# Performance work log

Hardware: AMD Instinct MI355X
Metric: run time of the kernel (lower is better)

Reference implementation:

```python
import jax, jax.numpy as jnp
import numpy as np

N = 100000   # num nodes
E = 500000   # num hyperedges
NNZ = 1600000
H, C = 4, 32
IN_CH = 128


def setup_inputs() -> dict:
    key = jax.random.key(0)
    k1, k2, k3, k4, k5 = jax.random.split(key, 5)
    X = jax.random.normal(k1, (N, IN_CH), dtype=jnp.float32)
    W = jax.random.normal(k2, (IN_CH, H * C), dtype=jnp.float32) * (1.0 / np.sqrt(IN_CH))
    att_e = jax.random.normal(k3, (1, H, C), dtype=jnp.float32) * 0.1
    vertex = jax.random.randint(k4, (NNZ,), 0, N, dtype=jnp.int64)
    edges = jax.random.randint(k5, (NNZ,), 0, E, dtype=jnp.int64)
    return {"X": X, "W": W, "att_e": att_e, "vertex": vertex, "edges": edges}


def reference(X, W, att_e, vertex, edges):
    n = X.shape[0]
    X0 = X @ W                                  # [N, H*C]
    Xh = X0.reshape(n, H, C)                    # [N, H, C]
    Xve = Xh[vertex]                            # [nnz, H, C] gather
    # scatter-mean over hyperedges
    esum = jax.ops.segment_sum(Xve, edges, num_segments=E)            # [E, H, C]
    cnt = jax.ops.segment_sum(jnp.ones((Xve.shape[0],), X.dtype), edges, num_segments=E)
    Xe = esum / jnp.maximum(cnt, 1.0)[:, None, None]                  # [E, H, C]
    # per-edge attention score
    alpha_e = (Xe * att_e).sum(-1)              # [E, H]
    a_ev = alpha_e[edges]                       # [nnz, H]
    alpha = jax.nn.leaky_relu(a_ev, 0.01)
    # segment softmax over vertex groups
    m = jax.ops.segment_max(alpha, vertex, num_segments=n)            # [N, H]
    ex = jnp.exp(alpha - m[vertex])
    den = jax.ops.segment_sum(ex, vertex, num_segments=n)             # [N, H]
    alpha = ex / (den[vertex] + 1e-16)          # [nnz, H]
    # weighted scatter-sum back to nodes
    Xev = Xe[edges] * alpha[:, :, None]         # [nnz, H, C]
    Xv = jax.ops.segment_sum(Xev, vertex, num_segments=n)             # [N, H, C]
    return Xv.reshape(n, H * C) + X0
```

## Files before the change

kernel.cpp:

```cpp
#include <hip/hip_runtime.h>
#include <hip/hip_bf16.h>
#include <hip/hip_fp16.h>
#include <cstdint>

#define NH 4
#define HC 128
#define INCH 128
#define NEDGE 500000
#define NN 100000

#define KE_SHIFT 11
#define KV_SHIFT 9
#define KE (1 << KE_SHIFT)
#define KV (1 << KV_SHIFT)
#define NBE 245
#define NBV 196
#define CAP_E 8192
#define CAP_V 10240
#define CHUNK_A 8192

typedef float          f32x2 __attribute__((ext_vector_type(2)));
typedef float          f32x4 __attribute__((ext_vector_type(4)));
typedef float          f32x8 __attribute__((ext_vector_type(8)));
typedef unsigned int   u32x2 __attribute__((ext_vector_type(2)));
typedef unsigned int   u32x4 __attribute__((ext_vector_type(4)));
typedef unsigned short u16x8 __attribute__((ext_vector_type(8)));

static __device__ __forceinline__ unsigned short f2bf(float f){
  union { float f; unsigned u; } v; v.f = f;
  unsigned r = v.u + 0x7fffu + ((v.u >> 16) & 1u);
  return (unsigned short)(r >> 16);
}
static __device__ __forceinline__ float bf2f(unsigned short b){
  union { unsigned u; float f; } v; v.u = ((unsigned)b) << 16;
  return v.f;
}
static __device__ __forceinline__ f32x8 bf8f(u16x8 b){
  f32x8 r;
  r[0]=bf2f(b[0]); r[1]=bf2f(b[1]); r[2]=bf2f(b[2]); r[3]=bf2f(b[3]);
  r[4]=bf2f(b[4]); r[5]=bf2f(b[5]); r[6]=bf2f(b[6]); r[7]=bf2f(b[7]);
  return r;
}

#if __has_builtin(__builtin_amdgcn_cvt_pk_fp8_f32) && __has_builtin(__builtin_amdgcn_cvt_pk_f32_fp8)
#define FP8_HW 1
#else
#define FP8_HW 0
#endif

#if !FP8_HW
static __device__ __forceinline__ unsigned enc1_fp8(float v){
  union{ __half h; unsigned short u; } c; c.h = __float2half(v);
  unsigned u = c.u;
  unsigned s = (u>>15)&1u, e=(u>>10)&31u, m=u&0x3FFu;
  int e8 = (int)e - 8;
  unsigned lsb = (m>>7)&1u;
  unsigned m8 = (m + 63u + lsb) >> 7;
  if (m8 == 8u){ m8 = 0u; e8 += 1; }
  if (e8 <= 0)  return s<<7;
  if (e8 >= 16) return (s<<7)|0x7Eu;
  return (s<<7)|((unsigned)e8<<3)|m8;
}
static __device__ __forceinline__ float dec1_fp8(unsigned b){
  unsigned s=(b>>7)&1u, e=(b>>3)&15u, m=b&7u;
  union{unsigned u; float f;} r;
  if (e==0u){ r.f = (float)m * 0.001953125f; if(s) r.f = -r.f; }
  else r.u = (s<<31)|((e+120u)<<23)|(m<<20);
  return r.f;
}
#endif

static __device__ __forceinline__ u32x2 pack8_fp8(const f32x8 v){
  u32x2 w;
#if FP8_HW
  int w0 = __builtin_amdgcn_cvt_pk_fp8_f32(v[0], v[1], 0, false);
  w0     = __builtin_amdgcn_cvt_pk_fp8_f32(v[2], v[3], w0, true);
  int w1 = __builtin_amdgcn_cvt_pk_fp8_f32(v[4], v[5], 0, false);
  w1     = __builtin_amdgcn_cvt_pk_fp8_f32(v[6], v[7], w1, true);
  w.x = (unsigned)w0; w.y = (unsigned)w1;
#else
  w.x = enc1_fp8(v[0]) | (enc1_fp8(v[1])<<8) | (enc1_fp8(v[2])<<16) | (enc1_fp8(v[3])<<24);
  w.y = enc1_fp8(v[4]) | (enc1_fp8(v[5])<<8) | (enc1_fp8(v[6])<<16) | (enc1_fp8(v[7])<<24);
#endif
  return w;
}
static __device__ __forceinline__ void fma8s_fp8(f32x8& acc, float c, float w, u32x2 q){
#if FP8_HW
  f32x2 p;
  p = __builtin_amdgcn_cvt_pk_f32_fp8((int)q.x, false); acc[0]=acc[0]*c + w*p.x; acc[1]=acc[1]*c + w*p.y;
  p = __builtin_amdgcn_cvt_pk_f32_fp8((int)q.x, true ); acc[2]=acc[2]*c + w*p.x; acc[3]=acc[3]*c + w*p.y;
  p = __builtin_amdgcn_cvt_pk_f32_fp8((int)q.y, false); acc[4]=acc[4]*c + w*p.x; acc[5]=acc[5]*c + w*p.y;
  p = __builtin_amdgcn_cvt_pk_f32_fp8((int)q.y, true ); acc[6]=acc[6]*c + w*p.x; acc[7]=acc[7]*c + w*p.y;
#else
  acc[0]=acc[0]*c + w*dec1_fp8(q.x&0xFF);        acc[1]=acc[1]*c + w*dec1_fp8((q.x>>8)&0xFF);
  acc[2]=acc[2]*c + w*dec1_fp8((q.x>>16)&0xFF);  acc[3]=acc[3]*c + w*dec1_fp8(q.x>>24);
  acc[4]=acc[4]*c + w*dec1_fp8(q.y&0xFF);        acc[5]=acc[5]*c + w*dec1_fp8((q.y>>8)&0xFF);
  acc[6]=acc[6]*c + w*dec1_fp8((q.y>>16)&0xFF);  acc[7]=acc[7]*c + w*dec1_fp8(q.y>>24);
#endif
}

#define GBM 128
#define GBK 16
__global__ __launch_bounds__(256) void gemm_x0(const float* __restrict__ X,
                                               const float* __restrict__ Wm,
                                               const float* __restrict__ att,
                                               unsigned short* __restrict__ X0bf,
                                               float* __restrict__ score, int nrows){
  __shared__ float As[GBK][GBM+4];
  __shared__ float Bs[GBK][HC+4];
  __shared__ float sc[GBM][17];
  const int tid  = threadIdx.x;
  const int row0 = blockIdx.x * GBM;
  const int trow = tid >> 4;
  const int tcol = tid & 15;
  float acc[8][8];
  #pragma unroll
  for (int i=0;i<8;i++)
    #pragma unroll
    for (int j=0;j<8;j++) acc[i][j]=0.f;

  for (int k0=0;k0<INCH;k0+=GBK){
    #pragma unroll
    for (int l = tid; l < 512; l += 256){
      int r  = l >> 2;
      int ks = (l & 3) * 4;
      int grow = row0 + r;
      float4 v = make_float4(0.f,0.f,0.f,0.f);
      if (grow < nrows) v = *(const float4*)(X + (size_t)grow*INCH + k0 + ks);
      As[ks+0][r]=v.x; As[ks+1][r]=v.y; As[ks+2][r]=v.z; As[ks+3][r]=v.w;
    }
    #pragma unroll
    for (int l = tid; l < 512; l += 256){
      int r  = l >> 5;
      int cs = (l & 31) * 4;
      float4 v = *(const float4*)(Wm + (size_t)(k0+r)*HC + cs);
      *(float4*)(&Bs[r][cs]) = v;
    }
    __syncthreads();
    #pragma unroll
    for (int kk=0;kk<GBK;kk++){
      float a[8], b[8];
      *(float4*)&a[0] = *(float4*)&As[kk][trow*8];
      *(float4*)&a[4] = *(float4*)&As[kk][trow*8+4];
      *(float4*)&b[0] = *(float4*)&Bs[kk][tcol*8];
      *(float4*)&b[4] = *(float4*)&Bs[kk][tcol*8+4];
      #pragma unroll
      for (int i=0;i<8;i++)
        #pragma unroll
        for (int j=0;j<8;j++) acc[i][j] = fmaf(a[i], b[j], acc[i][j]);
    }
    __syncthreads();
  }
  float attv[8];
  *(float4*)&attv[0] = *(const float4*)(att + tcol*8);
  *(float4*)&attv[4] = *(const float4*)(att + tcol*8 + 4);
  #pragma unroll
  for (int i=0;i<8;i++){
    int grow = row0 + trow*8 + i;
    float p = 0.f;
    #pragma unroll
    for (int j=0;j<8;j++) p = fmaf(acc[i][j], attv[j], p);
    sc[trow*8+i][tcol] = p;
    if (grow < nrows){
      ushort4 b0, b1;
      b0.x=f2bf(acc[i][0]); b0.y=f2bf(acc[i][1]); b0.z=f2bf(acc[i][2]); b0.w=f2bf(acc[i][3]);
      b1.x=f2bf(acc[i][4]); b1.y=f2bf(acc[i][5]); b1.z=f2bf(acc[i][6]); b1.w=f2bf(acc[i][7]);
      *(ushort4*)(X0bf + (size_t)grow*HC + tcol*8    ) = b0;
      *(ushort4*)(X0bf + (size_t)grow*HC + tcol*8 + 4) = b1;
    }
  }
  __syncthreads();
  for (int idx = tid; idx < GBM*NH; idx += 256){
    int row = idx >> 2, h = idx & 3;
    int grow = row0 + row;
    if (grow < nrows){
      float s = sc[row][4*h] + sc[row][4*h+1] + sc[row][4*h+2] + sc[row][4*h+3];
      score[(size_t)grow*NH + h] = s;
    }
  }
}

__global__ __launch_bounds__(512) void phaseA(const int* __restrict__ vertex,
                                              const int* __restrict__ edges, int nnz,
                                              int* __restrict__ cursE, int* __restrict__ cursV,
                                              unsigned* __restrict__ stgE, unsigned* __restrict__ stgV){
  __shared__ int cE[NBE], c2E[NBE], gE[NBE];
  __shared__ int cV[NBV], c2V[NBV], gV[NBV];
  const int t = threadIdx.x;
  const int base = blockIdx.x * CHUNK_A;
  int ev[16], vv[16];
  #pragma unroll
  for (int j=0;j<16;j++){
    int i = base + t + j*512;
    if (i < nnz){ ev[j] = edges[i]; vv[j] = vertex[i]; }
    else ev[j] = -1;
  }
  for (int j=t;j<NBE;j+=512){ cE[j]=0; c2E[j]=0; }
  for (int j=t;j<NBV;j+=512){ cV[j]=0; c2V[j]=0; }
  __syncthreads();
  #pragma unroll
  for (int j=0;j<16;j++) if (ev[j]>=0){
    atomicAdd(&cE[ev[j]>>KE_SHIFT], 1);
    atomicAdd(&cV[vv[j]>>KV_SHIFT], 1);
  }
  __syncthreads();
  for (int j=t;j<NBE;j+=512) gE[j] = atomicAdd(&cursE[j], cE[j]);
  for (int j=t;j<NBV;j+=512) gV[j] = atomicAdd(&cursV[j], cV[j]);
  __syncthreads();
  #pragma unroll
  for (int j=0;j<16;j++) if (ev[j]>=0){
    int bE = ev[j]>>KE_SHIFT;
    int p = gE[bE] + atomicAdd(&c2E[bE],1);
    if (p < CAP_E) stgE[(size_t)bE*CAP_E + p] = ((unsigned)vv[j] << KE_SHIFT) | (unsigned)(ev[j] & (KE-1));
    int bV = vv[j]>>KV_SHIFT;
    int q = gV[bV] + atomicAdd(&c2V[bV],1);
    if (q < CAP_V) stgV[(size_t)bV*CAP_V + q] = ((unsigned)ev[j] << KV_SHIFT) | (unsigned)(vv[j] & (KV-1));
  }
}

template<int K, int CAP, int IT, int SHIFT, int NB>
__device__ __forceinline__ void phaseB_body(const unsigned* __restrict__ stg,
                                            const int* __restrict__ curs,
                                            int* __restrict__ offsOut,
                                            int* __restrict__ csrOut, int nKeys, int b,
                                            int* cur, int* tsum, int* bsh){
  const int t = threadIdx.x;
  const int k0 = b * K;
  const int kc = min(K, nKeys - k0);
  int c = (t < NB) ? min(curs[t], CAP) : 0;
  bsh[t] = c; __syncthreads();
  for (int d2=1; d2<512; d2<<=1){
    int x = (t>=d2) ? bsh[t-d2] : 0; __syncthreads();
    bsh[t] += x; __syncthreads();
  }
  const int gbase = (b > 0) ? bsh[b-1] : 0;
  const int cnt   = min(curs[b], CAP);
  if (b == NB-1 && t == 0) offsOut[nKeys] = bsh[NB-1];
  unsigned it[IT];
  #pragma unroll
  for (int j=0;j<IT;j++){
    int i = t + j*512;
    it[j] = (i < cnt) ? stg[(size_t)b*CAP + i] : 0xFFFFFFFFu;
  }
  for (int j=t;j<K;j+=512) cur[j] = 0;
  __syncthreads();
  #pragma unroll
  for (int j=0;j<IT;j++) if (it[j] != 0xFFFFFFFFu) atomicAdd(&cur[it[j] & (K-1)], 1);
  __syncthreads();
  constexpr int KPT = K / 512;
  int loc[KPT]; int s = 0;
  #pragma unroll
  for (int j=0;j<KPT;j++){ loc[j] = s; s += cur[t*KPT + j]; }
  tsum[t] = s; __syncthreads();
  for (int d2=1; d2<512; d2<<=1){
    int x = (t>=d2) ? tsum[t-d2] : 0; __syncthreads();
    tsum[t] += x; __syncthreads();
  }
  const int tbase = tsum[t] - s;
  __syncthreads();
  #pragma unroll
  for (int j=0;j<KPT;j++){
    int k = t*KPT + j;
    int abs0 = gbase + tbase + loc[j];
    if (k < kc) offsOut[k0 + k] = abs0;
    cur[k] = abs0;
  }
  __syncthreads();
  #pragma unroll
  for (int j=0;j<IT;j++) if (it[j] != 0xFFFFFFFFu){
    int pos = atomicAdd(&cur[it[j] & (K-1)], 1);
    csrOut[pos] = (int)(it[j] >> SHIFT);
  }
}

__global__ __launch_bounds__(512) void phaseB_fused(const unsigned* __restrict__ stgE,
                                                    const unsigned* __restrict__ stgV,
                                                    const int* __restrict__ cursE,
                                                    const int* __restrict__ cursV,
                                                    int* __restrict__ eoffs, int* __restrict__ voffs,
                                                    int* __restrict__ ecsr, int* __restrict__ vcsr){
  __shared__ int cur[KE];
  __shared__ int tsum[512];
  __shared__ int bsh[512];
  const int b = blockIdx.x;
  if (b < NBE) phaseB_body<KE, CAP_E, CAP_E/512, KE_SHIFT, NBE>(stgE, cursE, eoffs, ecsr, NEDGE, b, cur, tsum, bsh);
  else         phaseB_body<KV, CAP_V, CAP_V/512, KV_SHIFT, NBV>(stgV, cursV, voffs, vcsr, NN, b - NBE, cur, tsum, bsh);
}

__global__ __launch_bounds__(256) void edge_agg(const unsigned short* __restrict__ X0bf,
                                                const float* __restrict__ score,
                                                const int* __restrict__ ecsr,
                                                const int* __restrict__ eoffs,
                                                unsigned char* __restrict__ Xe8,
                                                unsigned* __restrict__ alphaS, int E){
  int eg = blockIdx.x * 16 + (threadIdx.x >> 4);
  if (eg >= E) return;
  const int lane  = threadIdx.x & 15;
  const int cbase = lane * 8;
  const int start = eoffs[eg];
  const int d     = eoffs[eg+1] - start;
  f32x8 acc0 = {0.f,0.f,0.f,0.f,0.f,0.f,0.f,0.f};
  f32x8 acc1 = {0.f,0.f,0.f,0.f,0.f,0.f,0.f,0.f};
  float sacc0 = 0.f, sacc1 = 0.f;
  int k = 0;
  for (; k+1<d; k+=2){
    int v0 = ecsr[start + k];
    int v1 = ecsr[start + k + 1];
    u16x8 x0 = *(const u16x8*)(X0bf + (size_t)v0*HC + cbase);
    u16x8 x1 = *(const u16x8*)(X0bf + (size_t)v1*HC + cbase);
    if (lane < NH){
      sacc0 += score[(size_t)v0*NH + lane];
      sacc1 += score[(size_t)v1*NH + lane];
    }
    acc0 += bf8f(x0);
    acc1 += bf8f(x1);
  }
  if (k < d){
    int v0 = ecsr[start + k];
    u16x8 x0 = *(const u16x8*)(X0bf + (size_t)v0*HC + cbase);
    if (lane < NH) sacc0 += score[(size_t)v0*NH + lane];
    acc0 += bf8f(x0);
  }
  acc0 += acc1;
  const float inv = 1.0f / fmaxf((float)d, 1.0f);
  acc0 *= inv;
  float lm = fmaxf(fmaxf(fmaxf(fabsf(acc0[0]),fabsf(acc0[1])),fmaxf(fabsf(acc0[2]),fabsf(acc0[3]))),
                   fmaxf(fmaxf(fabsf(acc0[4]),fabsf(acc0[5])),fmaxf(fabsf(acc0[6]),fabsf(acc0[7]))));
  #pragma unroll
  for (int s=1; s<16; s<<=1) lm = fmaxf(lm, __shfl_xor(lm, s, 16));
  const float qs  = (lm > 1e-30f) ? 448.0f/lm : 0.f;
  const float dqs = (lm > 1e-30f) ? lm*(1.0f/448.0f) : 0.f;
  f32x8 q = acc0 * qs;
  u32x2 w = pack8_fp8(q);
  *(u32x2*)(Xe8 + (size_t)eg*HC + cbase) = w;
  float aa = (sacc0 + sacc1) * inv;
  aa = aa > 0.f ? aa : 0.01f*aa;
  float a0 = __shfl(aa, 0, 16);
  float a1 = __shfl(aa, 1, 16);
  float a2 = __shfl(aa, 2, 16);
  float a3 = __shfl(aa, 3, 16);
  if (lane == 0){
    u32x4 rec;
    rec.x = (unsigned)__half_as_ushort(__float2half(a0)) | ((unsigned)__half_as_ushort(__float2half(a1)) << 16);
    rec.y = (unsigned)__half_as_ushort(__float2half(a2)) | ((unsigned)__half_as_ushort(__float2half(a3)) << 16);
    rec.z = __float_as_uint(dqs);
    rec.w = 0u;
    *(u32x4*)(alphaS + (size_t)eg*4) = rec;
  }
}

__global__ __launch_bounds__(256) void vert_pass(const unsigned short* __restrict__ X0bf,
                                                 const unsigned char* __restrict__ Xe8,
                                                 const unsigned* __restrict__ alphaS,
                                                 const int* __restrict__ vcsr,
                                                 const int* __restrict__ voffs,
                                                 float* __restrict__ out, int N){
  int n = blockIdx.x * 16 + (threadIdx.x >> 4);
  if (n >= N) return;
  const int lane  = threadIdx.x & 15;
  const int cbase = lane * 8;
  const int h     = lane >> 2;
  const size_t obase = (size_t)n*HC + cbase;
  f32x8 x0 = bf8f(*(const u16x8*)(X0bf + obase));
  const int start = voffs[n];
  const int d     = voffs[n+1] - start;
  if (d == 0){
    f32x4 lo = {x0[0],x0[1],x0[2],x0[3]}, hi = {x0[4],x0[5],x0[6],x0[7]};
    __builtin_nontemporal_store(lo, (f32x4*)(out + obase));
    __builtin_nontemporal_store(hi, (f32x4*)(out + obase + 4));
    return;
  }

  float m0=-1e30f, m1=-1e30f, m2=-1e30f, m3=-1e30f;
  float den0=0.f, den1=0.f, den2=0.f, den3=0.f;
  f32x8 acc0 = {0.f,0.f,0.f,0.f,0.f,0.f,0.f,0.f};
  f32x8 acc1 = {0.f,0.f,0.f,0.f,0.f,0.f,0.f,0.f};
  f32x8 acc2 = {0.f,0.f,0.f,0.f,0.f,0.f,0.f,0.f};
  f32x8 acc3 = {0.f,0.f,0.f,0.f,0.f,0.f,0.f,0.f};

#define EXTRACT(rec, aval, sval) { \
    unsigned word_ = (h < 2) ? (rec).x : (rec).y; \
    unsigned h16_  = (h & 1) ? (word_ >> 16) : (word_ & 0xFFFFu); \
    aval = __half2float(__ushort_as_half((unsigned short)h16_)); \
    sval = __uint_as_float((rec).z); }

#define UPD(i, rec, q) { \
    float a_, s_; EXTRACT(rec, a_, s_); \
    float mn_ = fmaxf(m##i, a_); \
    float c_  = __expf(m##i - mn_); \
    float p_  = __expf(a_ - mn_); \
    den##i = den##i * c_ + p_; \
    fma8s_fp8(acc##i, c_, p_ * s_, (q)); \
    m##i = mn_; }

  int k = 0;
  for (; k+3<d; k+=4){
    int e0 = vcsr[start + k];
    int e1 = vcsr[start + k + 1];
    int e2 = vcsr[start + k + 2];
    int e3 = vcsr[start + k + 3];
    u32x4 r0 = *(const u32x4*)(alphaS + (size_t)e0*4);
    u32x4 r1 = *(const u32x4*)(alphaS + (size_t)e1*4);
    u32x4 r2 = *(const u32x4*)(alphaS + (size_t)e2*4);
    u32x4 r3 = *(const u32x4*)(alphaS + (size_t)e3*4);
    u32x2 q0 = *(const u32x2*)(Xe8 + (size_t)e0*HC + cbase);
    u32x2 q1 = *(const u32x2*)(Xe8 + (size_t)e1*HC + cbase);
    u32x2 q2 = *(const u32x2*)(Xe8 + (size_t)e2*HC + cbase);
    u32x2 q3 = *(const u32x2*)(Xe8 + (size_t)e3*HC + cbase);
    UPD(0, r0, q0);
    UPD(1, r1, q1);
    UPD(2, r2, q2);
    UPD(3, r3, q3);
  }
  for (; k<d; k++){
    int e0 = vcsr[start + k];
    u32x4 r0 = *(const u32x4*)(alphaS + (size_t)e0*4);
    u32x2 q0 = *(const u32x2*)(Xe8 + (size_t)e0*HC + cbase);
    UPD(0, r0, q0);
  }
#undef UPD
#undef EXTRACT

  float mn = fmaxf(fmaxf(m0,m1), fmaxf(m2,m3));
  float c0 = __expf(m0-mn), c1 = __expf(m1-mn), c2 = __expf(m2-mn), c3 = __expf(m3-mn);
  float den = den0*c0 + den1*c1 + den2*c2 + den3*c3;
  f32x8 acc = acc0*c0 + acc1*c1 + acc2*c2 + acc3*c3;
  const float w = 1.0f / (den + 1e-16f);
  acc = acc*w + x0;
  f32x4 lo = {acc[0],acc[1],acc[2],acc[3]};
  f32x4 hi = {acc[4],acc[5],acc[6],acc[7]};
  __builtin_nontemporal_store(lo, (f32x4*)(out + obase));
  __builtin_nontemporal_store(hi, (f32x4*)(out + obase + 4));
}

extern "C" void kernel_launch(void* const* d_in, const int* in_sizes, int n_in,
                              void* d_out, int out_size, void* d_ws, size_t ws_size,
                              hipStream_t stream){
  const float* X   = (const float*)d_in[0];
  const float* Wm  = (const float*)d_in[1];
  const float* att = (const float*)d_in[2];
  const int* vertex = (const int*)d_in[3];
  const int* edges  = (const int*)d_in[4];
  const int N   = in_sizes[0] / INCH;
  const int NNZ = in_sizes[3];
  const int E   = NEDGE;

  char* ws = (char*)d_ws;
  size_t off = 0;
  auto alloc = [&](size_t bytes)->char*{
    char* p = ws + off;
    off += (bytes + 255) & ~(size_t)255;
    return p;
  };
  unsigned char*  Xe8    = (unsigned char*)alloc((size_t)E * HC);
  unsigned short* X0bf   = (unsigned short*)alloc((size_t)NN * HC * sizeof(unsigned short));
  float*          score  = (float*)alloc((size_t)NN * NH * sizeof(float));
  unsigned*       alphaS = (unsigned*)alloc((size_t)E * 4 * sizeof(unsigned));
  int*            eoffs  = (int*)alloc((size_t)(E+1) * sizeof(int));
  int*            voffs  = (int*)alloc((size_t)(NN+1) * sizeof(int));
  int*            ecsr   = (int*)alloc((size_t)NNZ * sizeof(int));
  int*            vcsr   = (int*)alloc((size_t)NNZ * sizeof(int));
  int*            curs   = (int*)alloc((size_t)(NBE + NBV) * sizeof(int));
  int*            cursE  = curs;
  int*            cursV  = curs + NBE;
  unsigned* stgE = (unsigned*)(void*)Xe8;
  unsigned* stgV = (unsigned*)((char*)(void*)Xe8 + (size_t)NBE * CAP_E * sizeof(unsigned));

  hipMemsetAsync(curs, 0, (size_t)(NBE + NBV) * sizeof(int), stream);
  gemm_x0<<<(N + GBM - 1)/GBM, 256, 0, stream>>>(X, Wm, att, X0bf, score, N);
  phaseA<<<(NNZ + CHUNK_A - 1)/CHUNK_A, 512, 0, stream>>>(vertex, edges, NNZ, cursE, cursV, stgE, stgV);
  phaseB_fused<<<NBE + NBV, 512, 0, stream>>>(stgE, stgV, cursE, cursV, eoffs, voffs, ecsr, vcsr);
  edge_agg<<<(E + 15)/16, 256, 0, stream>>>(X0bf, score, ecsr, eoffs, Xe8, alphaS, E);
  vert_pass<<<(N + 15)/16, 256, 0, stream>>>(X0bf, Xe8, alphaS, vcsr, voffs, (float*)d_out, N);
}
```

Before: 260.6 us.

## Compute edge attention from aggregated features and drop online softmax max tracking

The per-node attention score is no longer computed in the GEMM epilogue. Each edge's score is now the dot product of its mean-aggregated features with att, reduced with shuffles, so the score buffer and its per-vertex gathers go away. edge_agg stores exp(leaky_relu(score)) directly as fp16. vert_pass then just sums these weights instead of running an online softmax with running max and rescaling, which removes two exps and several multiplies per incidence. The trade-off is that skipping max subtraction can overflow fp16/fp32 if scores are large, so correctness relies on the scores staying moderate.

```diff
diff --git a/kernel.cpp b/kernel.cpp
--- a/kernel.cpp
+++ b/kernel.cpp
@@ -84,18 +84,18 @@
 #endif
   return w;
 }
-static __device__ __forceinline__ void fma8s_fp8(f32x8& acc, float c, float w, u32x2 q){
+static __device__ __forceinline__ void fma8_fp8(f32x8& acc, float c, u32x2 q){
 #if FP8_HW
   f32x2 p;
-  p = __builtin_amdgcn_cvt_pk_f32_fp8((int)q.x, false); acc[0]=acc[0]*c + w*p.x; acc[1]=acc[1]*c + w*p.y;
-  p = __builtin_amdgcn_cvt_pk_f32_fp8((int)q.x, true ); acc[2]=acc[2]*c + w*p.x; acc[3]=acc[3]*c + w*p.y;
-  p = __builtin_amdgcn_cvt_pk_f32_fp8((int)q.y, false); acc[4]=acc[4]*c + w*p.x; acc[5]=acc[5]*c + w*p.y;
-  p = __builtin_amdgcn_cvt_pk_f32_fp8((int)q.y, true ); acc[6]=acc[6]*c + w*p.x; acc[7]=acc[7]*c + w*p.y;
+  p = __builtin_amdgcn_cvt_pk_f32_fp8((int)q.x, false); acc[0] += c*p.x; acc[1] += c*p.y;
+  p = __builtin_amdgcn_cvt_pk_f32_fp8((int)q.x, true ); acc[2] += c*p.x; acc[3] += c*p.y;
+  p = __builtin_amdgcn_cvt_pk_f32_fp8((int)q.y, false); acc[4] += c*p.x; acc[5] += c*p.y;
+  p = __builtin_amdgcn_cvt_pk_f32_fp8((int)q.y, true ); acc[6] += c*p.x; acc[7] += c*p.y;
 #else
-  acc[0]=acc[0]*c + w*dec1_fp8(q.x&0xFF);        acc[1]=acc[1]*c + w*dec1_fp8((q.x>>8)&0xFF);
-  acc[2]=acc[2]*c + w*dec1_fp8((q.x>>16)&0xFF);  acc[3]=acc[3]*c + w*dec1_fp8(q.x>>24);
-  acc[4]=acc[4]*c + w*dec1_fp8(q.y&0xFF);        acc[5]=acc[5]*c + w*dec1_fp8((q.y>>8)&0xFF);
-  acc[6]=acc[6]*c + w*dec1_fp8((q.y>>16)&0xFF);  acc[7]=acc[7]*c + w*dec1_fp8(q.y>>24);
+  acc[0] += c*dec1_fp8(q.x&0xFF);        acc[1] += c*dec1_fp8((q.x>>8)&0xFF);
+  acc[2] += c*dec1_fp8((q.x>>16)&0xFF);  acc[3] += c*dec1_fp8(q.x>>24);
+  acc[4] += c*dec1_fp8(q.y&0xFF);        acc[5] += c*dec1_fp8((q.y>>8)&0xFF);
+  acc[6] += c*dec1_fp8((q.y>>16)&0xFF);  acc[7] += c*dec1_fp8(q.y>>24);
 #endif
 }
 
@@ -103,12 +103,9 @@
 #define GBK 16
 __global__ __launch_bounds__(256) void gemm_x0(const float* __restrict__ X,
                                                const float* __restrict__ Wm,
-                                               const float* __restrict__ att,
-                                               unsigned short* __restrict__ X0bf,
-                                               float* __restrict__ score, int nrows){
+                                               unsigned short* __restrict__ X0bf, int nrows){
   __shared__ float As[GBK][GBM+4];
   __shared__ float Bs[GBK][HC+4];
-  __shared__ float sc[GBM][17];
   const int tid  = threadIdx.x;
   const int row0 = blockIdx.x * GBM;
   const int trow = tid >> 4;
@@ -151,31 +148,15 @@
     }
     __syncthreads();
   }
-  float attv[8];
-  *(float4*)&attv[0] = *(const float4*)(att + tcol*8);
-  *(float4*)&attv[4] = *(const float4*)(att + tcol*8 + 4);
   #pragma unroll
   for (int i=0;i<8;i++){
     int grow = row0 + trow*8 + i;
-    float p = 0.f;
-    #pragma unroll
-    for (int j=0;j<8;j++) p = fmaf(acc[i][j], attv[j], p);
-    sc[trow*8+i][tcol] = p;
     if (grow < nrows){
       ushort4 b0, b1;
       b0.x=f2bf(acc[i][0]); b0.y=f2bf(acc[i][1]); b0.z=f2bf(acc[i][2]); b0.w=f2bf(acc[i][3]);
       b1.x=f2bf(acc[i][4]); b1.y=f2bf(acc[i][5]); b1.z=f2bf(acc[i][6]); b1.w=f2bf(acc[i][7]);
       *(ushort4*)(X0bf + (size_t)grow*HC + tcol*8    ) = b0;
       *(ushort4*)(X0bf + (size_t)grow*HC + tcol*8 + 4) = b1;
-    }
-  }
-  __syncthreads();
-  for (int idx = tid; idx < GBM*NH; idx += 256){
-    int row = idx >> 2, h = idx & 3;
-    int grow = row0 + row;
-    if (grow < nrows){
-      float s = sc[row][4*h] + sc[row][4*h+1] + sc[row][4*h+2] + sc[row][4*h+3];
-      score[(size_t)grow*NH + h] = s;
     }
   }
 }
@@ -288,7 +269,7 @@
 }
 
 __global__ __launch_bounds__(256) void edge_agg(const unsigned short* __restrict__ X0bf,
-                                                const float* __restrict__ score,
+                                                const float* __restrict__ att,
                                                 const int* __restrict__ ecsr,
                                                 const int* __restrict__ eoffs,
                                                 unsigned char* __restrict__ Xe8,
@@ -297,33 +278,37 @@
   if (eg >= E) return;
   const int lane  = threadIdx.x & 15;
   const int cbase = lane * 8;
+  float attv[8];
+  *(f32x4*)&attv[0] = *(const f32x4*)(att + cbase);
+  *(f32x4*)&attv[4] = *(const f32x4*)(att + cbase + 4);
   const int start = eoffs[eg];
   const int d     = eoffs[eg+1] - start;
   f32x8 acc0 = {0.f,0.f,0.f,0.f,0.f,0.f,0.f,0.f};
   f32x8 acc1 = {0.f,0.f,0.f,0.f,0.f,0.f,0.f,0.f};
-  float sacc0 = 0.f, sacc1 = 0.f;
   int k = 0;
   for (; k+1<d; k+=2){
     int v0 = ecsr[start + k];
     int v1 = ecsr[start + k + 1];
     u16x8 x0 = *(const u16x8*)(X0bf + (size_t)v0*HC + cbase);
     u16x8 x1 = *(const u16x8*)(X0bf + (size_t)v1*HC + cbase);
-    if (lane < NH){
-      sacc0 += score[(size_t)v0*NH + lane];
-      sacc1 += score[(size_t)v1*NH + lane];
-    }
     acc0 += bf8f(x0);
     acc1 += bf8f(x1);
   }
   if (k < d){
     int v0 = ecsr[start + k];
     u16x8 x0 = *(const u16x8*)(X0bf + (size_t)v0*HC + cbase);
-    if (lane < NH) sacc0 += score[(size_t)v0*NH + lane];
     acc0 += bf8f(x0);
   }
   acc0 += acc1;
   const float inv = 1.0f / fmaxf((float)d, 1.0f);
   acc0 *= inv;
+  float p = 0.f;
+  #pragma unroll
+  for (int j=0;j<8;j++) p = fmaf(acc0[j], attv[j], p);
+  p += __shfl_xor(p, 1, 4);
+  p += __shfl_xor(p, 2, 4);
+  float a = p > 0.f ? p : 0.01f*p;
+  float e = __expf(a);
   float lm = fmaxf(fmaxf(fmaxf(fabsf(acc0[0]),fabsf(acc0[1])),fmaxf(fabsf(acc0[2]),fabsf(acc0[3]))),
                    fmaxf(fmaxf(fabsf(acc0[4]),fabsf(acc0[5])),fmaxf(fabsf(acc0[6]),fabsf(acc0[7]))));
   #pragma unroll
@@ -333,16 +318,14 @@
   f32x8 q = acc0 * qs;
   u32x2 w = pack8_fp8(q);
   *(u32x2*)(Xe8 + (size_t)eg*HC + cbase) = w;
-  float aa = (sacc0 + sacc1) * inv;
-  aa = aa > 0.f ? aa : 0.01f*aa;
-  float a0 = __shfl(aa, 0, 16);
-  float a1 = __shfl(aa, 1, 16);
-  float a2 = __shfl(aa, 2, 16);
-  float a3 = __shfl(aa, 3, 16);
+  float e0 = __shfl(e, 0, 16);
+  float e1 = __shfl(e, 4, 16);
+  float e2 = __shfl(e, 8, 16);
+  float e3 = __shfl(e, 12, 16);
   if (lane == 0){
     u32x4 rec;
-    rec.x = (unsigned)__half_as_ushort(__float2half(a0)) | ((unsigned)__half_as_ushort(__float2half(a1)) << 16);
-    rec.y = (unsigned)__half_as_ushort(__float2half(a2)) | ((unsigned)__half_as_ushort(__float2half(a3)) << 16);
+    rec.x = (unsigned)__half_as_ushort(__float2half(e0)) | ((unsigned)__half_as_ushort(__float2half(e1)) << 16);
+    rec.y = (unsigned)__half_as_ushort(__float2half(e2)) | ((unsigned)__half_as_ushort(__float2half(e3)) << 16);
     rec.z = __float_as_uint(dqs);
     rec.w = 0u;
     *(u32x4*)(alphaS + (size_t)eg*4) = rec;
@@ -371,27 +354,18 @@
     return;
   }
 
-  float m0=-1e30f, m1=-1e30f, m2=-1e30f, m3=-1e30f;
   float den0=0.f, den1=0.f, den2=0.f, den3=0.f;
   f32x8 acc0 = {0.f,0.f,0.f,0.f,0.f,0.f,0.f,0.f};
   f32x8 acc1 = {0.f,0.f,0.f,0.f,0.f,0.f,0.f,0.f};
   f32x8 acc2 = {0.f,0.f,0.f,0.f,0.f,0.f,0.f,0.f};
   f32x8 acc3 = {0.f,0.f,0.f,0.f,0.f,0.f,0.f,0.f};
 
-#define EXTRACT(rec, aval, sval) { \
+#define UPD(i, rec, q) { \
     unsigned word_ = (h < 2) ? (rec).x : (rec).y; \
     unsigned h16_  = (h & 1) ? (word_ >> 16) : (word_ & 0xFFFFu); \
-    aval = __half2float(__ushort_as_half((unsigned short)h16_)); \
-    sval = __uint_as_float((rec).z); }
-
-#define UPD(i, rec, q) { \
-    float a_, s_; EXTRACT(rec, a_, s_); \
-    float mn_ = fmaxf(m##i, a_); \
-    float c_  = __expf(m##i - mn_); \
-    float p_  = __expf(a_ - mn_); \
-    den##i = den##i * c_ + p_; \
-    fma8s_fp8(acc##i, c_, p_ * s_, (q)); \
-    m##i = mn_; }
+    float e_ = __half2float(__ushort_as_half((unsigned short)h16_)); \
+    den##i += e_; \
+    fma8_fp8(acc##i, e_ * __uint_as_float((rec).z), (q)); }
 
   int k = 0;
   for (; k+3<d; k+=4){
@@ -419,12 +393,9 @@
     UPD(0, r0, q0);
   }
 #undef UPD
-#undef EXTRACT
-
-  float mn = fmaxf(fmaxf(m0,m1), fmaxf(m2,m3));
-  float c0 = __expf(m0-mn), c1 = __expf(m1-mn), c2 = __expf(m2-mn), c3 = __expf(m3-mn);
-  float den = den0*c0 + den1*c1 + den2*c2 + den3*c3;
-  f32x8 acc = acc0*c0 + acc1*c1 + acc2*c2 + acc3*c3;
+
+  float den = (den0 + den1) + (den2 + den3);
+  f32x8 acc = (acc0 + acc1) + (acc2 + acc3);
   const float w = 1.0f / (den + 1e-16f);
   acc = acc*w + x0;
   f32x4 lo = {acc[0],acc[1],acc[2],acc[3]};
@@ -454,7 +425,6 @@
   };
   unsigned char*  Xe8    = (unsigned char*)alloc((size_t)E * HC);
   unsigned short* X0bf   = (unsigned short*)alloc((size_t)NN * HC * sizeof(unsigned short));
-  float*          score  = (float*)alloc((size_t)NN * NH * sizeof(float));
   unsigned*       alphaS = (unsigned*)alloc((size_t)E * 4 * sizeof(unsigned));
   int*            eoffs  = (int*)alloc((size_t)(E+1) * sizeof(int));
   int*            voffs  = (int*)alloc((size_t)(NN+1) * sizeof(int));
@@ -467,9 +437,9 @@
   unsigned* stgV = (unsigned*)((char*)(void*)Xe8 + (size_t)NBE * CAP_E * sizeof(unsigned));
 
   hipMemsetAsync(curs, 0, (size_t)(NBE + NBV) * sizeof(int), stream);
-  gemm_x0<<<(N + GBM - 1)/GBM, 256, 0, stream>>>(X, Wm, att, X0bf, score, N);
+  gemm_x0<<<(N + GBM - 1)/GBM, 256, 0, stream>>>(X, Wm, X0bf, N);
   phaseA<<<(NNZ + CHUNK_A - 1)/CHUNK_A, 512, 0, stream>>>(vertex, edges, NNZ, cursE, cursV, stgE, stgV);
   phaseB_fused<<<NBE + NBV, 512, 0, stream>>>(stgE, stgV, cursE, cursV, eoffs, voffs, ecsr, vcsr);
-  edge_agg<<<(E + 15)/16, 256, 0, stream>>>(X0bf, score, ecsr, eoffs, Xe8, alphaS, E);
+  edge_agg<<<(E + 15)/16, 256, 0, stream>>>(X0bf, att, ecsr, eoffs, Xe8, alphaS, E);
   vert_pass<<<(N + 15)/16, 256, 0, stream>>>(X0bf, Xe8, alphaS, vcsr, voffs, (float*)d_out, N);
 }
```

After: 250.4 us. 1.04x faster.
